# Optimization experiments

Hardware: AMD Instinct MI355X
Metric: run time of the kernel (lower is better)

## Reference

```python
import jax, jax.numpy as jnp
import numpy as np

B, F, E = 4096, 39, 16
FIELD_DIMS = [1000] * F
OFFSETS = jnp.asarray(np.concatenate([[0], np.cumsum(FIELD_DIMS)[:-1]]).astype(np.int64))
I_IDX, J_IDX = np.triu_indices(F, 1)  # 741 pairs (i<j)
I_IDX = jnp.asarray(I_IDX); J_IDX = jnp.asarray(J_IDX)
MLP_DIMS = [2 * 741 * E, 400, 400, 400]
EPS = 1e-5


def setup_inputs() -> dict:
    key = jax.random.key(0)
    ks = jax.random.split(key, 20)
    s = 0.02
    inp = {
        'x': jax.random.randint(ks[0], (B, F), 0, 1000, dtype=jnp.int64),
        'emb': jax.random.normal(ks[1], (sum(FIELD_DIMS), E), jnp.float32) * s,
        'sen_w1': jax.random.normal(ks[2], (F, F), jnp.float32) * s,
        'sen_b1': jnp.zeros((F,), jnp.float32),
        'sen_w2': jax.random.normal(ks[3], (F, F), jnp.float32) * s,
        'sen_b2': jnp.zeros((F,), jnp.float32),
        'Wb1': jax.random.normal(ks[4], (E, E), jnp.float32) * s,
        'Wb2': jax.random.normal(ks[5], (E, E), jnp.float32) * s,
    }
    for li in range(3):
        din, dout = MLP_DIMS[li], MLP_DIMS[li + 1]
        inp[f'mw{li}'] = jax.random.normal(ks[6 + li], (dout, din), jnp.float32) * s
        inp[f'mb{li}'] = jnp.zeros((dout,), jnp.float32)
        inp[f'g{li}'] = jnp.ones((dout,), jnp.float32)
        inp[f'be{li}'] = jnp.zeros((dout,), jnp.float32)
    inp['mw3'] = jax.random.normal(ks[9], (1, MLP_DIMS[-1]), jnp.float32) * s
    inp['mb3'] = jnp.zeros((1,), jnp.float32)
    return inp


def _bilinear_all(v, W):
    # v: [B,F,E]; p_ij = (v_i W^T) * v_j for all i<j -> [B, P*E]
    proj = jnp.einsum('bfe,de->bfd', v, W)
    p = proj[:, I_IDX] * v[:, J_IDX]  # [B, 741, E]
    return p.reshape(v.shape[0], -1)


def _bn(h, g, be):
    mu = h.mean(axis=0)
    var = h.var(axis=0)
    return g * (h - mu) * jax.lax.rsqrt(var + EPS) + be


def _forward(x, emb, sen_w1, sen_b1, sen_w2, sen_b2, Wb1, Wb2,
             mw0, mb0, g0, be0, mw1, mb1, g1, be1, mw2, mb2, g2, be2, mw3, mb3):
    xe = emb[x + OFFSETS[None, :]]  # [B,F,E]
    # SENet: max over embed dim, two-layer excitation with ReLU
    z = jnp.max(xe, axis=2)  # [B,F]
    a = jax.nn.relu(jax.nn.relu(z @ sen_w1.T + sen_b1) @ sen_w2.T + sen_b2)  # [B,F]
    x_sen = a[:, :, None] * xe
    x_con = jnp.concatenate([_bilinear_all(xe, Wb1), _bilinear_all(x_sen, Wb2)], axis=1)
    h = x_con
    for w, b, g, be in ((mw0, mb0, g0, be0), (mw1, mb1, g1, be1), (mw2, mb2, g2, be2)):
        h = jax.nn.relu(_bn(h @ w.T + b, g, be))  # dropout = identity (eval)
    return h @ mw3.T + mb3  # [B,1]


def reference(x, emb, sen_w1, sen_b1, sen_w2, sen_b2, Wb1, Wb2,
              mw0, mb0, g0, be0, mw1, mb1, g1, be1, mw2, mb2, g2, be2, mw3, mb3):
    return _forward(x, emb, sen_w1, sen_b1, sen_w2, sen_b2, Wb1, Wb2,
                    mw0, mb0, g0, be0, mw1, mb1, g1, be1, mw2, mb2, g2, be2, mw3, mb3)
```

## Files before the change

kernel.cpp:

```cpp
#include <hip/hip_runtime.h>
#include <stdint.h>

#define B_ROWS  4096
#define F_FIELDS 39
#define NPAIR   741
#define XCON_K  23712
#define KP      23744
#define NP      512
#define HID     400
#define SPLITK0 8
#define KITERS0 (KP/64)

#define OFF_XCON 0ull
#define SZ_XCON  ((size_t)B_ROWS * KP * 2)
#define OFF_W0B  (OFF_XCON + SZ_XCON)
#define SZ_W0B   ((size_t)NP * KP * 2)
#define OFF_W1B  (OFF_W0B + SZ_W0B)
#define SZ_WSM   ((size_t)NP * NP * 2)
#define OFF_W2B  (OFF_W1B + SZ_WSM)
#define OFF_HPRE (OFF_W2B + SZ_WSM)
#define SZ_HPRE  ((size_t)B_ROWS * NP * 4)
#define OFF_HN   (OFF_HPRE + SZ_HPRE)
#define SZ_HN    ((size_t)B_ROWS * NP * 2)
#define OFF_STATS (OFF_HN + SZ_HN)
#define SZ_STATS  (6 * 512 * 4)
#define WS_NEEDED (OFF_STATS + SZ_STATS + 4096)

__device__ __forceinline__ unsigned short f2bf(float f) {
    union { float f; unsigned u; } v; v.f = f;
    unsigned r = (v.u + 0x7FFFu + ((v.u >> 16) & 1u)) >> 16;
    return (unsigned short)r;
}
__device__ __forceinline__ float bf2f(unsigned short h) {
    union { unsigned u; float f; } v; v.u = ((unsigned)h) << 16;
    return v.f;
}
__device__ __forceinline__ void gl_lds16(const void* g, void* l) {
    __builtin_amdgcn_global_load_lds(
        (const __attribute__((address_space(1))) void*)g,
        (__attribute__((address_space(3))) void*)l, 16, 0, 0);
}

typedef __bf16 bf16x8 __attribute__((ext_vector_type(8)));
typedef float  floatx4 __attribute__((ext_vector_type(4)));

__global__ __launch_bounds__(256) void build_all(
    const int* __restrict__ x, const float* __restrict__ emb,
    const float* __restrict__ w1, const float* __restrict__ b1,
    const float* __restrict__ w2, const float* __restrict__ b2,
    const float* __restrict__ Wb1, const float* __restrict__ Wb2,
    unsigned short* __restrict__ xcon,
    const float* __restrict__ mw0, unsigned short* __restrict__ w0b,
    const float* __restrict__ mw1, const float* __restrict__ mw2,
    unsigned short* __restrict__ w1b, unsigned short* __restrict__ w2b)
{
    __shared__ float xe[624], p0[624], sp[624], sx[624];
    __shared__ float zz[40], tt[40], aa[40];
    __shared__ short itab[NPAIR], jtab[NPAIR];
    const int bb = blockIdx.x, tid = threadIdx.x;

    if (bb >= B_ROWS) {
        if (bb < B_ROWS + NP) {
            const int o = bb - B_ROWS;
            for (int k4 = tid; k4 < KP / 4; k4 += 256) {
                const int k = k4 * 4;
                unsigned short u[4] = {0, 0, 0, 0};
                if (o < HID && k < XCON_K) {
                    float4 v = *(const float4*)&mw0[(size_t)o * XCON_K + k];
                    u[0] = f2bf(v.x); u[1] = f2bf(v.y); u[2] = f2bf(v.z); u[3] = f2bf(v.w);
                }
                uint2 pk; pk.x = u[0] | ((unsigned)u[1] << 16); pk.y = u[2] | ((unsigned)u[3] << 16);
                *(uint2*)&w0b[(size_t)o * KP + k] = pk;
            }
        } else {
            const int idx = bb - B_ROWS - NP;
            const int which = idx >> 9;
            const int o = idx & 511;
            const float* w = which ? mw2 : mw1;
            unsigned short* o_ = which ? w2b : w1b;
            for (int k = tid; k < NP; k += 256) {
                float v = (o < HID && k < HID) ? w[o * HID + k] : 0.f;
                o_[o * NP + k] = f2bf(v);
            }
        }
        return;
    }

    const int b = bb;
    for (int p = tid; p < NPAIR; p += 256) {
        float fp = (float)p;
        int i = (int)(38.5f - sqrtf(38.5f * 38.5f - 2.f * fp));
        while (i > 0 && p < (i * (77 - i)) / 2) --i;
        while (p >= ((i + 1) * (76 - i)) / 2) ++i;
        itab[p] = (short)i;
        jtab[p] = (short)(i + 1 + (p - (i * (77 - i)) / 2));
    }
    if (tid < 156) {
        int f = tid >> 2, e4 = (tid & 3) * 4;
        int row = x[b * F_FIELDS + f] + 1000 * f;
        *(float4*)&xe[f * 16 + e4] = *(const float4*)&emb[row * 16 + e4];
    }
    __syncthreads();
    if (tid < F_FIELDS) {
        float m = xe[tid * 16];
        for (int e = 1; e < 16; ++e) m = fmaxf(m, xe[tid * 16 + e]);
        zz[tid] = m;
    }
    __syncthreads();
    if (tid < F_FIELDS) {
        float s = b1[tid];
        for (int g = 0; g < F_FIELDS; ++g) s += zz[g] * w1[tid * F_FIELDS + g];
        tt[tid] = fmaxf(s, 0.f);
    }
    __syncthreads();
    if (tid < F_FIELDS) {
        float s = b2[tid];
        for (int g = 0; g < F_FIELDS; ++g) s += tt[g] * w2[tid * F_FIELDS + g];
        aa[tid] = fmaxf(s, 0.f);
    }
    __syncthreads();
    for (int idx = tid; idx < 624; idx += 256) {
        int f = idx >> 4, d = idx & 15;
        float s1 = 0.f, s2 = 0.f;
        for (int e = 0; e < 16; ++e) {
            float v = xe[f * 16 + e];
            s1 += v * Wb1[d * 16 + e];
            s2 += v * Wb2[d * 16 + e];
        }
        const float af = aa[f];
        p0[idx] = s1;
        sp[idx] = af * s2;
        sx[idx] = af * xe[idx];
    }
    __syncthreads();
    unsigned short* out = xcon + (size_t)b * KP;
    for (int c = tid; c < 1484; c += 256) {
        if (c < 2 * NPAIR) {
            const int half = (c >= NPAIR);
            const int p = c - NPAIR * half;
            const int i = itab[p], j = jtab[p];
            const float* pr = half ? &sp[i * 16] : &p0[i * 16];
            const float* xr = half ? &sx[j * 16] : &xe[j * 16];
            unsigned short u[16];
#pragma unroll
            for (int q = 0; q < 4; ++q) {
                float4 a = *(const float4*)(pr + q * 4);
                float4 bx = *(const float4*)(xr + q * 4);
                u[q * 4 + 0] = f2bf(a.x * bx.x);
                u[q * 4 + 1] = f2bf(a.y * bx.y);
                u[q * 4 + 2] = f2bf(a.z * bx.z);
                u[q * 4 + 3] = f2bf(a.w * bx.w);
            }
            uint4 v0, v1;
            v0.x = u[0] | ((unsigned)u[1] << 16);  v0.y = u[2] | ((unsigned)u[3] << 16);
            v0.z = u[4] | ((unsigned)u[5] << 16);  v0.w = u[6] | ((unsigned)u[7] << 16);
            v1.x = u[8] | ((unsigned)u[9] << 16);  v1.y = u[10] | ((unsigned)u[11] << 16);
            v1.z = u[12] | ((unsigned)u[13] << 16); v1.w = u[14] | ((unsigned)u[15] << 16);
            uint4* dst = (uint4*)(out + (half ? 11856 : 0) + p * 16);
            dst[0] = v0; dst[1] = v1;
        } else {
            uint4 z; z.x = z.y = z.z = z.w = 0u;
            ((uint4*)(out + XCON_K))[c - 2 * NPAIR] = z;
        }
    }
}

__global__ __launch_bounds__(256, 2) void gemm0(
    const unsigned short* __restrict__ A, const unsigned short* __restrict__ Bm,
    float* __restrict__ C, int kcnt)
{
    __shared__ __align__(16) unsigned short As[128 * 64];
    __shared__ __align__(16) unsigned short Bs[256 * 64];
    const int tid = threadIdx.x;
    const int m0 = blockIdx.y * 128, n0 = blockIdx.x * 256;
    int kb = blockIdx.z * kcnt;
    int ke = kb + kcnt; if (ke > KITERS0) ke = KITERS0;

    const int swz = (((tid & 7) ^ ((tid >> 3) & 7)) * 8);
    const unsigned short* Ag = A + (size_t)(m0 + (tid >> 3)) * KP + swz;
    const unsigned short* Bg = Bm + (size_t)(n0 + (tid >> 3)) * KP + swz;
    unsigned short* Asl = As + tid * 8;
    unsigned short* Bsl = Bs + tid * 8;

    const int wv = tid >> 6, ln = tid & 63;
    const int wm = (wv >> 1) * 64, wn = (wv & 1) * 128;
    const int l15 = ln & 15, lq = ln >> 4;
    const int xorm = l15 & 7;

    floatx4 acc[4][8];
#pragma unroll
    for (int mi = 0; mi < 4; ++mi)
#pragma unroll
        for (int ni = 0; ni < 8; ++ni)
            acc[mi][ni] = (floatx4){0.f, 0.f, 0.f, 0.f};

    for (int kt = kb; kt < ke; ++kt) {
        const size_t ko = (size_t)kt * 64;
#pragma unroll
        for (int i = 0; i < 4; ++i)
            gl_lds16(Ag + (size_t)(i * 32) * KP + ko, Asl + i * 2048);
#pragma unroll
        for (int i = 0; i < 8; ++i)
            gl_lds16(Bg + (size_t)(i * 32) * KP + ko, Bsl + i * 2048);
        __syncthreads();
#pragma unroll
        for (int kk = 0; kk < 64; kk += 32) {
            bf16x8 af[4], bfr[8];
#pragma unroll
            for (int t = 0; t < 4; ++t)
                af[t] = *(const bf16x8*)(As + (wm + t * 16 + l15) * 64
                                            + ((((kk >> 3) + lq) ^ xorm) * 8));
#pragma unroll
            for (int t = 0; t < 8; ++t)
                bfr[t] = *(const bf16x8*)(Bs + (wn + t * 16 + l15) * 64
                                             + ((((kk >> 3) + lq) ^ xorm) * 8));
#pragma unroll
            for (int mi = 0; mi < 4; ++mi)
#pragma unroll
                for (int ni = 0; ni < 8; ++ni)
                    acc[mi][ni] = __builtin_amdgcn_mfma_f32_16x16x32_bf16(
                        af[mi], bfr[ni], acc[mi][ni], 0, 0, 0);
        }
        __syncthreads();
    }
#pragma unroll
    for (int mi = 0; mi < 4; ++mi)
#pragma unroll
        for (int ni = 0; ni < 8; ++ni) {
            const int col = n0 + wn + ni * 16 + l15;
            const int row0 = m0 + wm + mi * 16 + lq * 4;
#pragma unroll
            for (int r = 0; r < 4; ++r)
                atomicAdd(&C[(size_t)(row0 + r) * NP + col], acc[mi][ni][r]);
        }
}

template<int MODE>
__global__ __launch_bounds__(256) void gemm_bn(
    const void* __restrict__ Ain, const unsigned short* __restrict__ Bm,
    const float* __restrict__ cs, const float* __restrict__ csq,
    const float* __restrict__ g, const float* __restrict__ be,
    void* __restrict__ Cout, float* __restrict__ csO, float* __restrict__ csqO)
{
    __shared__ __align__(16) unsigned short As[64 * 64];
    __shared__ __align__(16) unsigned short Bs[64 * 64];
    __shared__ float sc[NP], sh[NP];
    const int tid = threadIdx.x;
    const int m0 = blockIdx.y * 64, n0 = blockIdx.x * 64;

    for (int c = tid; c < NP; c += 256) {
        float mean = cs[c] * (1.f / 4096.f);
        float var  = csq[c] * (1.f / 4096.f) - mean * mean;
        float s = (c < HID ? g[c] : 0.f) * rsqrtf(var + 1e-5f);
        sc[c] = s;
        sh[c] = (c < HID ? be[c] : 0.f) - mean * s;
    }

    const int r = tid >> 3, c8 = tid & 7;
    const int gsw = c8 ^ (r & 7);
    const unsigned short* Bg = Bm + (size_t)(n0 + r) * NP + gsw * 8;
    unsigned short* Bsl = Bs + tid * 8;

    const int wv = tid >> 6, ln = tid & 63;
    const int wm = (wv >> 1) * 32, wn = (wv & 1) * 32;
    const int l15 = ln & 15, lq = ln >> 4;
    const int xorm = l15 & 7;

    floatx4 acc[2][2];
#pragma unroll
    for (int mi = 0; mi < 2; ++mi)
#pragma unroll
        for (int ni = 0; ni < 2; ++ni)
            acc[mi][ni] = (floatx4){0.f, 0.f, 0.f, 0.f};

    __syncthreads();

    for (int kt = 0; kt < NP / 64; ++kt) {
        const int ko = kt * 64;
        const int kc = ko + gsw * 8;
#pragma unroll
        for (int i = 0; i < 2; ++i) {
            const int row = m0 + r + i * 32;
            unsigned short u[8];
            if (MODE == 0) {
                const float* ap = (const float*)Ain + (size_t)row * NP + kc;
                float4 v0 = *(const float4*)ap;
                float4 v1 = *(const float4*)(ap + 4);
                u[0] = f2bf(fmaxf(v0.x * sc[kc]     + sh[kc],     0.f));
                u[1] = f2bf(fmaxf(v0.y * sc[kc + 1] + sh[kc + 1], 0.f));
                u[2] = f2bf(fmaxf(v0.z * sc[kc + 2] + sh[kc + 2], 0.f));
                u[3] = f2bf(fmaxf(v0.w * sc[kc + 3] + sh[kc + 3], 0.f));
                u[4] = f2bf(fmaxf(v1.x * sc[kc + 4] + sh[kc + 4], 0.f));
                u[5] = f2bf(fmaxf(v1.y * sc[kc + 5] + sh[kc + 5], 0.f));
                u[6] = f2bf(fmaxf(v1.z * sc[kc + 6] + sh[kc + 6], 0.f));
                u[7] = f2bf(fmaxf(v1.w * sc[kc + 7] + sh[kc + 7], 0.f));
            } else {
                const unsigned short* ap = (const unsigned short*)Ain + (size_t)row * NP + kc;
                uint4 pk = *(const uint4*)ap;
                unsigned short raw[8] = {
                    (unsigned short)(pk.x & 0xFFFF), (unsigned short)(pk.x >> 16),
                    (unsigned short)(pk.y & 0xFFFF), (unsigned short)(pk.y >> 16),
                    (unsigned short)(pk.z & 0xFFFF), (unsigned short)(pk.z >> 16),
                    (unsigned short)(pk.w & 0xFFFF), (unsigned short)(pk.w >> 16)};
#pragma unroll
                for (int e = 0; e < 8; ++e)
                    u[e] = f2bf(fmaxf(bf2f(raw[e]) * sc[kc + e] + sh[kc + e], 0.f));
            }
            uint4 w;
            w.x = u[0] | ((unsigned)u[1] << 16);
            w.y = u[2] | ((unsigned)u[3] << 16);
            w.z = u[4] | ((unsigned)u[5] << 16);
            w.w = u[6] | ((unsigned)u[7] << 16);
            *(uint4*)(As + (r + i * 32) * 64 + c8 * 8) = w;
        }
#pragma unroll
        for (int i = 0; i < 2; ++i)
            gl_lds16(Bg + (size_t)(i * 32) * NP + ko, Bsl + i * 2048);
        __syncthreads();
#pragma unroll
        for (int kk = 0; kk < 64; kk += 32) {
            bf16x8 af[2], bfr[2];
#pragma unroll
            for (int t = 0; t < 2; ++t) {
                af[t]  = *(const bf16x8*)(As + (wm + t * 16 + l15) * 64
                                             + ((((kk >> 3) + lq) ^ xorm) * 8));
                bfr[t] = *(const bf16x8*)(Bs + (wn + t * 16 + l15) * 64
                                             + ((((kk >> 3) + lq) ^ xorm) * 8));
            }
#pragma unroll
            for (int mi = 0; mi < 2; ++mi)
#pragma unroll
                for (int ni = 0; ni < 2; ++ni)
                    acc[mi][ni] = __builtin_amdgcn_mfma_f32_16x16x32_bf16(
                        af[mi], bfr[ni], acc[mi][ni], 0, 0, 0);
        }
        __syncthreads();
    }
#pragma unroll
    for (int mi = 0; mi < 2; ++mi)
#pragma unroll
        for (int ni = 0; ni < 2; ++ni) {
            const int col = n0 + wn + ni * 16 + l15;
            const int row0 = m0 + wm + mi * 16 + lq * 4;
#pragma unroll
            for (int rr = 0; rr < 4; ++rr) {
                if (MODE == 0)
                    ((unsigned short*)Cout)[(size_t)(row0 + rr) * NP + col] = f2bf(acc[mi][ni][rr]);
                else
                    ((float*)Cout)[(size_t)(row0 + rr) * NP + col] = acc[mi][ni][rr];
            }
        }
#pragma unroll
    for (int ni = 0; ni < 2; ++ni) {
        float s = 0.f, q = 0.f;
#pragma unroll
        for (int mi = 0; mi < 2; ++mi)
#pragma unroll
            for (int rr = 0; rr < 4; ++rr) { float v = acc[mi][ni][rr]; s += v; q += v * v; }
        s += __shfl_down(s, 32); q += __shfl_down(q, 32);
        s += __shfl_down(s, 16); q += __shfl_down(q, 16);
        if (lq == 0) {
            const int col = n0 + wn + ni * 16 + l15;
            atomicAdd(&csO[col], s);
            atomicAdd(&csqO[col], q);
        }
    }
}

__global__ __launch_bounds__(256) void colstats(const float* __restrict__ H,
                                                float* __restrict__ cs, float* __restrict__ csq) {
    const int tid = threadIdx.x;
    const int c4 = (tid & 127) * 4;
    const int ro = tid >> 7;
    const int r0 = blockIdx.x * 32;
    float s0 = 0, s1 = 0, s2 = 0, s3 = 0, q0 = 0, q1 = 0, q2 = 0, q3 = 0;
#pragma unroll
    for (int i = 0; i < 16; ++i) {
        float4 v = *(const float4*)&H[(size_t)(r0 + ro + 2 * i) * NP + c4];
        s0 += v.x; q0 += v.x * v.x;  s1 += v.y; q1 += v.y * v.y;
        s2 += v.z; q2 += v.z * v.z;  s3 += v.w; q3 += v.w * v.w;
    }
    atomicAdd(&cs[c4], s0); atomicAdd(&cs[c4 + 1], s1);
    atomicAdd(&cs[c4 + 2], s2); atomicAdd(&cs[c4 + 3], s3);
    atomicAdd(&csq[c4], q0); atomicAdd(&csq[c4 + 1], q1);
    atomicAdd(&csq[c4 + 2], q2); atomicAdd(&csq[c4 + 3], q3);
}

__global__ __launch_bounds__(256) void bnrelu_dot(const float* __restrict__ H,
                       const float* __restrict__ cs, const float* __restrict__ csq,
                       const float* __restrict__ g, const float* __restrict__ be,
                       const float* __restrict__ w3, const float* __restrict__ b3,
                       float* __restrict__ out) {
    __shared__ float sc[NP], sh[NP], ww[NP];
    for (int c = threadIdx.x; c < NP; c += 256) {
        float mean = cs[c] * (1.f / 4096.f);
        float var  = csq[c] * (1.f / 4096.f) - mean * mean;
        float s = (c < HID ? g[c] : 0.f) * rsqrtf(var + 1e-5f);
        sc[c] = s;
        sh[c] = (c < HID ? be[c] : 0.f) - mean * s;
        ww[c] = (c < HID ? w3[c] : 0.f);
    }
    __syncthreads();
    const int wv = threadIdx.x >> 6, ln = threadIdx.x & 63;
    const int row = blockIdx.x * 4 + wv;
    const float4* hp = (const float4*)(H + (size_t)row * NP);
    float s = 0.f;
#pragma unroll
    for (int it = 0; it < 2; ++it) {
        const int c4 = it * 64 + ln;
        const int c = c4 * 4;
        float4 v = hp[c4];
        s += fmaxf(v.x * sc[c]     + sh[c],     0.f) * ww[c]
           + fmaxf(v.y * sc[c + 1] + sh[c + 1], 0.f) * ww[c + 1]
           + fmaxf(v.z * sc[c + 2] + sh[c + 2], 0.f) * ww[c + 2]
           + fmaxf(v.w * sc[c + 3] + sh[c + 3], 0.f) * ww[c + 3];
    }
#pragma unroll
    for (int o = 32; o; o >>= 1) s += __shfl_down(s, o);
    if (ln == 0) out[row] = s + b3[0];
}

extern "C" void kernel_launch(void* const* d_in, const int* in_sizes, int n_in,
                              void* d_out, int out_size, void* d_ws, size_t ws_size,
                              hipStream_t stream)
{
    const int*   x    = (const int*)d_in[0];
    const float* emb  = (const float*)d_in[1];
    const float* sw1  = (const float*)d_in[2];
    const float* sb1  = (const float*)d_in[3];
    const float* sw2  = (const float*)d_in[4];
    const float* sb2  = (const float*)d_in[5];
    const float* Wb1  = (const float*)d_in[6];
    const float* Wb2  = (const float*)d_in[7];
    const float* mw0  = (const float*)d_in[8];
    const float* g0   = (const float*)d_in[10];
    const float* be0  = (const float*)d_in[11];
    const float* mw1  = (const float*)d_in[12];
    const float* g1   = (const float*)d_in[14];
    const float* be1  = (const float*)d_in[15];
    const float* mw2  = (const float*)d_in[16];
    const float* g2   = (const float*)d_in[18];
    const float* be2  = (const float*)d_in[19];
    const float* mw3  = (const float*)d_in[20];
    const float* mb3  = (const float*)d_in[21];
    (void)in_sizes; (void)n_in; (void)out_size;
    if (ws_size < WS_NEEDED) return;

    char* ws = (char*)d_ws;
    unsigned short* xcon = (unsigned short*)(ws + OFF_XCON);
    unsigned short* w0b  = (unsigned short*)(ws + OFF_W0B);
    unsigned short* w1b  = (unsigned short*)(ws + OFF_W1B);
    unsigned short* w2b  = (unsigned short*)(ws + OFF_W2B);
    float* hpre = (float*)(ws + OFF_HPRE);
    unsigned short* hn = (unsigned short*)(ws + OFF_HN);
    float* stats = (float*)(ws + OFF_STATS);
    float* cs0 = stats,        *csq0 = stats + 512;
    float* cs1 = stats + 1024, *csq1 = stats + 1536;
    float* cs2 = stats + 2048, *csq2 = stats + 2560;

    build_all<<<B_ROWS + NP + 2 * NP, 256, 0, stream>>>(
        x, emb, sw1, sb1, sw2, sb2, Wb1, Wb2, xcon, mw0, w0b, mw1, mw2, w1b, w2b);

    hipMemsetAsync(hpre, 0, SZ_HPRE, stream);
    hipMemsetAsync(stats, 0, SZ_STATS, stream);

    gemm0<<<dim3(NP / 256, B_ROWS / 128, SPLITK0), 256, 0, stream>>>(
        xcon, w0b, hpre, (KITERS0 + SPLITK0 - 1) / SPLITK0);
    colstats<<<128, 256, 0, stream>>>(hpre, cs0, csq0);

    gemm_bn<0><<<dim3(NP / 64, B_ROWS / 64), 256, 0, stream>>>(
        hpre, w1b, cs0, csq0, g0, be0, hn, cs1, csq1);

    gemm_bn<1><<<dim3(NP / 64, B_ROWS / 64), 256, 0, stream>>>(
        hn, w2b, cs1, csq1, g1, be1, hpre, cs2, csq2);

    bnrelu_dot<<<B_ROWS / 4, 256, 0, stream>>>(hpre, cs2, csq2, g2, be2, mw3, mb3, (float*)d_out);
}
```

Before: 378.9 us.

## Write split-K partials to slabs and fuse reduction with column stats; pack rows per block

Split-K partial results of the first GEMM go to per-split slabs with plain stores, replacing the float atomics into a zeroed buffer. A new reduce_stats kernel sums the slabs, writes the result and accumulates the BN column statistics, so the hpre memset and separate colstats pass are dropped. The slab path only runs if the workspace is large enough and otherwise falls back to the old atomic path. Separately, build_all now handles four batch rows per block, one per wavefront, to cut block count and share the pair-index tables. The slabs add roughly 64MB of extra write and read traffic.

Result: slower. 403.4 us (+6.5%).

```diff
diff --git a/kernel.cpp b/kernel.cpp
--- a/kernel.cpp
+++ b/kernel.cpp
@@ -10,6 +10,7 @@
 #define HID     400
 #define SPLITK0 8
 #define KITERS0 (KP/64)
+#define NROWBLK (B_ROWS/4)
 
 #define OFF_XCON 0ull
 #define SZ_XCON  ((size_t)B_ROWS * KP * 2)
@@ -25,6 +26,10 @@
 #define OFF_STATS (OFF_HN + SZ_HN)
 #define SZ_STATS  (6 * 512 * 4)
 #define WS_NEEDED (OFF_STATS + SZ_STATS + 4096)
+#define OFF_PART  (OFF_STATS + SZ_STATS)
+#define SLAB_ELEMS ((size_t)B_ROWS * NP)
+#define SZ_PART   ((size_t)SPLITK0 * SLAB_ELEMS * 4)
+#define WS_BIG    (OFF_PART + SZ_PART + 4096)
 
 __device__ __forceinline__ unsigned short f2bf(float f) {
     union { float f; unsigned u; } v; v.f = f;
@@ -54,14 +59,11 @@
     const float* __restrict__ mw1, const float* __restrict__ mw2,
     unsigned short* __restrict__ w1b, unsigned short* __restrict__ w2b)
 {
-    __shared__ float xe[624], p0[624], sp[624], sx[624];
-    __shared__ float zz[40], tt[40], aa[40];
-    __shared__ short itab[NPAIR], jtab[NPAIR];
     const int bb = blockIdx.x, tid = threadIdx.x;
 
-    if (bb >= B_ROWS) {
-        if (bb < B_ROWS + NP) {
-            const int o = bb - B_ROWS;
+    if (bb >= NROWBLK) {
+        if (bb < NROWBLK + NP) {
+            const int o = bb - NROWBLK;
             for (int k4 = tid; k4 < KP / 4; k4 += 256) {
                 const int k = k4 * 4;
                 unsigned short u[4] = {0, 0, 0, 0};
@@ -73,7 +75,7 @@
                 *(uint2*)&w0b[(size_t)o * KP + k] = pk;
             }
         } else {
-            const int idx = bb - B_ROWS - NP;
+            const int idx = bb - NROWBLK - NP;
             const int which = idx >> 9;
             const int o = idx & 511;
             const float* w = which ? mw2 : mw1;
@@ -86,7 +88,12 @@
         return;
     }
 
-    const int b = bb;
+    __shared__ float xe[4][624], p0[4][624], sp[4][624], sx[4][624];
+    __shared__ float zz[4][40], tt[4][40], aa[4][40];
+    __shared__ short itab[NPAIR], jtab[NPAIR];
+    const int wv = tid >> 6, ln = tid & 63;
+    const int b = bb * 4 + wv;
+
     for (int p = tid; p < NPAIR; p += 256) {
         float fp = (float)p;
         int i = (int)(38.5f - sqrtf(38.5f * 38.5f - 2.f * fp));
@@ -95,52 +102,52 @@
         itab[p] = (short)i;
         jtab[p] = (short)(i + 1 + (p - (i * (77 - i)) / 2));
     }
-    if (tid < 156) {
-        int f = tid >> 2, e4 = (tid & 3) * 4;
+    for (int k = ln; k < 156; k += 64) {
+        int f = k >> 2, e4 = (k & 3) * 4;
         int row = x[b * F_FIELDS + f] + 1000 * f;
-        *(float4*)&xe[f * 16 + e4] = *(const float4*)&emb[row * 16 + e4];
-    }
-    __syncthreads();
-    if (tid < F_FIELDS) {
-        float m = xe[tid * 16];
-        for (int e = 1; e < 16; ++e) m = fmaxf(m, xe[tid * 16 + e]);
-        zz[tid] = m;
-    }
-    __syncthreads();
-    if (tid < F_FIELDS) {
-        float s = b1[tid];
-        for (int g = 0; g < F_FIELDS; ++g) s += zz[g] * w1[tid * F_FIELDS + g];
-        tt[tid] = fmaxf(s, 0.f);
-    }
-    __syncthreads();
-    if (tid < F_FIELDS) {
-        float s = b2[tid];
-        for (int g = 0; g < F_FIELDS; ++g) s += tt[g] * w2[tid * F_FIELDS + g];
-        aa[tid] = fmaxf(s, 0.f);
-    }
-    __syncthreads();
-    for (int idx = tid; idx < 624; idx += 256) {
+        *(float4*)&xe[wv][f * 16 + e4] = *(const float4*)&emb[row * 16 + e4];
+    }
+    __syncthreads();
+    if (ln < F_FIELDS) {
+        float m = xe[wv][ln * 16];
+        for (int e = 1; e < 16; ++e) m = fmaxf(m, xe[wv][ln * 16 + e]);
+        zz[wv][ln] = m;
+    }
+    __syncthreads();
+    if (ln < F_FIELDS) {
+        float s = b1[ln];
+        for (int g = 0; g < F_FIELDS; ++g) s += zz[wv][g] * w1[ln * F_FIELDS + g];
+        tt[wv][ln] = fmaxf(s, 0.f);
+    }
+    __syncthreads();
+    if (ln < F_FIELDS) {
+        float s = b2[ln];
+        for (int g = 0; g < F_FIELDS; ++g) s += tt[wv][g] * w2[ln * F_FIELDS + g];
+        aa[wv][ln] = fmaxf(s, 0.f);
+    }
+    __syncthreads();
+    for (int idx = ln; idx < 624; idx += 64) {
         int f = idx >> 4, d = idx & 15;
         float s1 = 0.f, s2 = 0.f;
         for (int e = 0; e < 16; ++e) {
-            float v = xe[f * 16 + e];
+            float v = xe[wv][f * 16 + e];
             s1 += v * Wb1[d * 16 + e];
             s2 += v * Wb2[d * 16 + e];
         }
-        const float af = aa[f];
-        p0[idx] = s1;
-        sp[idx] = af * s2;
-        sx[idx] = af * xe[idx];
+        const float af = aa[wv][f];
+        p0[wv][idx] = s1;
+        sp[wv][idx] = af * s2;
+        sx[wv][idx] = af * xe[wv][idx];
     }
     __syncthreads();
     unsigned short* out = xcon + (size_t)b * KP;
-    for (int c = tid; c < 1484; c += 256) {
+    for (int c = ln; c < 1484; c += 64) {
         if (c < 2 * NPAIR) {
             const int half = (c >= NPAIR);
             const int p = c - NPAIR * half;
             const int i = itab[p], j = jtab[p];
-            const float* pr = half ? &sp[i * 16] : &p0[i * 16];
-            const float* xr = half ? &sx[j * 16] : &xe[j * 16];
+            const float* pr = half ? &sp[wv][i * 16] : &p0[wv][i * 16];
+            const float* xr = half ? &sx[wv][j * 16] : &xe[wv][j * 16];
             unsigned short u[16];
 #pragma unroll
             for (int q = 0; q < 4; ++q) {
@@ -159,15 +166,15 @@
             uint4* dst = (uint4*)(out + (half ? 11856 : 0) + p * 16);
             dst[0] = v0; dst[1] = v1;
         } else {
-            uint4 z; z.x = z.y = z.z = z.w = 0u;
-            ((uint4*)(out + XCON_K))[c - 2 * NPAIR] = z;
+            uint4 z4; z4.x = z4.y = z4.z = z4.w = 0u;
+            ((uint4*)(out + XCON_K))[c - 2 * NPAIR] = z4;
         }
     }
 }
 
 __global__ __launch_bounds__(256, 2) void gemm0(
     const unsigned short* __restrict__ A, const unsigned short* __restrict__ Bm,
-    float* __restrict__ C, int kcnt)
+    float* __restrict__ C, float* __restrict__ Cslab, int kcnt, int use_slab)
 {
     __shared__ __align__(16) unsigned short As[128 * 64];
     __shared__ __align__(16) unsigned short Bs[256 * 64];
@@ -223,16 +230,75 @@
         }
         __syncthreads();
     }
-#pragma unroll
-    for (int mi = 0; mi < 4; ++mi)
-#pragma unroll
-        for (int ni = 0; ni < 8; ++ni) {
-            const int col = n0 + wn + ni * 16 + l15;
-            const int row0 = m0 + wm + mi * 16 + lq * 4;
-#pragma unroll
-            for (int r = 0; r < 4; ++r)
-                atomicAdd(&C[(size_t)(row0 + r) * NP + col], acc[mi][ni][r]);
-        }
+    if (use_slab) {
+        float* slab = Cslab + (size_t)blockIdx.z * SLAB_ELEMS;
+#pragma unroll
+        for (int mi = 0; mi < 4; ++mi)
+#pragma unroll
+            for (int ni = 0; ni < 8; ++ni) {
+                const int col = n0 + wn + ni * 16 + l15;
+                const int row0 = m0 + wm + mi * 16 + lq * 4;
+#pragma unroll
+                for (int r = 0; r < 4; ++r)
+                    slab[(size_t)(row0 + r) * NP + col] = acc[mi][ni][r];
+            }
+    } else {
+#pragma unroll
+        for (int mi = 0; mi < 4; ++mi)
+#pragma unroll
+            for (int ni = 0; ni < 8; ++ni) {
+                const int col = n0 + wn + ni * 16 + l15;
+                const int row0 = m0 + wm + mi * 16 + lq * 4;
+#pragma unroll
+                for (int r = 0; r < 4; ++r)
+                    atomicAdd(&C[(size_t)(row0 + r) * NP + col], acc[mi][ni][r]);
+            }
+    }
+}
+
+__global__ __launch_bounds__(256) void reduce_stats(const float* __restrict__ P,
+                        float* __restrict__ H, float* __restrict__ cs, float* __restrict__ csq) {
+    const int tid = threadIdx.x;
+    const int c4 = (tid & 127) * 4;
+    const int ro = tid >> 7;
+    const int r0 = blockIdx.x * 16;
+    float s0 = 0, s1 = 0, s2 = 0, s3 = 0, q0 = 0, q1 = 0, q2 = 0, q3 = 0;
+#pragma unroll
+    for (int i = 0; i < 8; ++i) {
+        const size_t off = (size_t)(r0 + ro + 2 * i) * NP + c4;
+        float4 a = *(const float4*)&P[off];
+#pragma unroll
+        for (int z = 1; z < SPLITK0; ++z) {
+            float4 b = *(const float4*)&P[(size_t)z * SLAB_ELEMS + off];
+            a.x += b.x; a.y += b.y; a.z += b.z; a.w += b.w;
+        }
+        *(float4*)&H[off] = a;
+        s0 += a.x; q0 += a.x * a.x;  s1 += a.y; q1 += a.y * a.y;
+        s2 += a.z; q2 += a.z * a.z;  s3 += a.w; q3 += a.w * a.w;
+    }
+    atomicAdd(&cs[c4], s0); atomicAdd(&cs[c4 + 1], s1);
+    atomicAdd(&cs[c4 + 2], s2); atomicAdd(&cs[c4 + 3], s3);
+    atomicAdd(&csq[c4], q0); atomicAdd(&csq[c4 + 1], q1);
+    atomicAdd(&csq[c4 + 2], q2); atomicAdd(&csq[c4 + 3], q3);
+}
+
+__global__ __launch_bounds__(256) void colstats(const float* __restrict__ H,
+                                                float* __restrict__ cs, float* __restrict__ csq) {
+    const int tid = threadIdx.x;
+    const int c4 = (tid & 127) * 4;
+    const int ro = tid >> 7;
+    const int r0 = blockIdx.x * 16;
+    float s0 = 0, s1 = 0, s2 = 0, s3 = 0, q0 = 0, q1 = 0, q2 = 0, q3 = 0;
+#pragma unroll
+    for (int i = 0; i < 8; ++i) {
+        float4 v = *(const float4*)&H[(size_t)(r0 + ro + 2 * i) * NP + c4];
+        s0 += v.x; q0 += v.x * v.x;  s1 += v.y; q1 += v.y * v.y;
+        s2 += v.z; q2 += v.z * v.z;  s3 += v.w; q3 += v.w * v.w;
+    }
+    atomicAdd(&cs[c4], s0); atomicAdd(&cs[c4 + 1], s1);
+    atomicAdd(&cs[c4 + 2], s2); atomicAdd(&cs[c4 + 3], s3);
+    atomicAdd(&csq[c4], q0); atomicAdd(&csq[c4 + 1], q1);
+    atomicAdd(&csq[c4 + 2], q2); atomicAdd(&csq[c4 + 3], q3);
 }
 
 template<int MODE>
@@ -365,25 +431,6 @@
             atomicAdd(&csqO[col], q);
         }
     }
-}
-
-__global__ __launch_bounds__(256) void colstats(const float* __restrict__ H,
-                                                float* __restrict__ cs, float* __restrict__ csq) {
-    const int tid = threadIdx.x;
-    const int c4 = (tid & 127) * 4;
-    const int ro = tid >> 7;
-    const int r0 = blockIdx.x * 32;
-    float s0 = 0, s1 = 0, s2 = 0, s3 = 0, q0 = 0, q1 = 0, q2 = 0, q3 = 0;
-#pragma unroll
-    for (int i = 0; i < 16; ++i) {
-        float4 v = *(const float4*)&H[(size_t)(r0 + ro + 2 * i) * NP + c4];
-        s0 += v.x; q0 += v.x * v.x;  s1 += v.y; q1 += v.y * v.y;
-        s2 += v.z; q2 += v.z * v.z;  s3 += v.w; q3 += v.w * v.w;
-    }
-    atomicAdd(&cs[c4], s0); atomicAdd(&cs[c4 + 1], s1);
-    atomicAdd(&cs[c4 + 2], s2); atomicAdd(&cs[c4 + 3], s3);
-    atomicAdd(&csq[c4], q0); atomicAdd(&csq[c4 + 1], q1);
-    atomicAdd(&csq[c4 + 2], q2); atomicAdd(&csq[c4 + 3], q3);
 }
 
 __global__ __launch_bounds__(256) void bnrelu_dot(const float* __restrict__ H,
@@ -445,6 +492,7 @@
     const float* mb3  = (const float*)d_in[21];
     (void)in_sizes; (void)n_in; (void)out_size;
     if (ws_size < WS_NEEDED) return;
+    const int use_slab = (ws_size >= WS_BIG) ? 1 : 0;
 
     char* ws = (char*)d_ws;
     unsigned short* xcon = (unsigned short*)(ws + OFF_XCON);
@@ -454,19 +502,26 @@
     float* hpre = (float*)(ws + OFF_HPRE);
     unsigned short* hn = (unsigned short*)(ws + OFF_HN);
     float* stats = (float*)(ws + OFF_STATS);
+    float* slab  = (float*)(ws + OFF_PART);
     float* cs0 = stats,        *csq0 = stats + 512;
     float* cs1 = stats + 1024, *csq1 = stats + 1536;
     float* cs2 = stats + 2048, *csq2 = stats + 2560;
 
-    build_all<<<B_ROWS + NP + 2 * NP, 256, 0, stream>>>(
+    build_all<<<NROWBLK + NP + 2 * NP, 256, 0, stream>>>(
         x, emb, sw1, sb1, sw2, sb2, Wb1, Wb2, xcon, mw0, w0b, mw1, mw2, w1b, w2b);
 
-    hipMemsetAsync(hpre, 0, SZ_HPRE, stream);
     hipMemsetAsync(stats, 0, SZ_STATS, stream);
 
-    gemm0<<<dim3(NP / 256, B_ROWS / 128, SPLITK0), 256, 0, stream>>>(
-        xcon, w0b, hpre, (KITERS0 + SPLITK0 - 1) / SPLITK0);
-    colstats<<<128, 256, 0, stream>>>(hpre, cs0, csq0);
+    if (use_slab) {
+        gemm0<<<dim3(NP / 256, B_ROWS / 128, SPLITK0), 256, 0, stream>>>(
+            xcon, w0b, hpre, slab, (KITERS0 + SPLITK0 - 1) / SPLITK0, 1);
+        reduce_stats<<<256, 256, 0, stream>>>(slab, hpre, cs0, csq0);
+    } else {
+        hipMemsetAsync(hpre, 0, SZ_HPRE, stream);
+        gemm0<<<dim3(NP / 256, B_ROWS / 128, SPLITK0), 256, 0, stream>>>(
+            xcon, w0b, hpre, slab, (KITERS0 + SPLITK0 - 1) / SPLITK0, 0);
+        colstats<<<256, 256, 0, stream>>>(hpre, cs0, csq0);
+    }
 
     gemm_bn<0><<<dim3(NP / 64, B_ROWS / 64), 256, 0, stream>>>(
         hpre, w1b, cs0, csq0, g0, be0, hn, cs1, csq1);
```

## Shrink gemm0 tile to 128x128, raise occupancy, split xcon stores per thread

Applied to the files above, without the earlier changes.

The main split-K GEMM tile shrinks from 128x256 to 128x128, with fewer accumulators per wave and launch bounds raised to 4 blocks per CU. The grid doubles in the N dimension, which should improve occupancy and load balance. In exchange each A tile is reloaded twice as often. The xcon build loop now has each thread write one 16-byte chunk, so stores are contiguous and the padding branch is folded in. colstats uses twice as many blocks, each covering half the rows.

New measurement: 424.1 us. 11.9% more time.

```diff
diff --git a/kernel.cpp b/kernel.cpp
--- a/kernel.cpp
+++ b/kernel.cpp
@@ -133,17 +133,20 @@
         sx[idx] = af * xe[idx];
     }
     __syncthreads();
-    unsigned short* out = xcon + (size_t)b * KP;
-    for (int c = tid; c < 1484; c += 256) {
-        if (c < 2 * NPAIR) {
-            const int half = (c >= NPAIR);
-            const int p = c - NPAIR * half;
+    uint4* out4 = (uint4*)(xcon + (size_t)b * KP);
+    for (int s = tid; s < 2968; s += 256) {
+        uint4 w;
+        if (s < 2964) {
+            const int p2 = s >> 1;
+            const int hi = s & 1;
+            const int half = (p2 >= NPAIR);
+            const int p = p2 - NPAIR * half;
             const int i = itab[p], j = jtab[p];
-            const float* pr = half ? &sp[i * 16] : &p0[i * 16];
-            const float* xr = half ? &sx[j * 16] : &xe[j * 16];
-            unsigned short u[16];
-#pragma unroll
-            for (int q = 0; q < 4; ++q) {
+            const float* pr = (half ? &sp[i * 16] : &p0[i * 16]) + hi * 8;
+            const float* xr = (half ? &sx[j * 16] : &xe[j * 16]) + hi * 8;
+            unsigned short u[8];
+#pragma unroll
+            for (int q = 0; q < 2; ++q) {
                 float4 a = *(const float4*)(pr + q * 4);
                 float4 bx = *(const float4*)(xr + q * 4);
                 u[q * 4 + 0] = f2bf(a.x * bx.x);
@@ -151,28 +154,25 @@
                 u[q * 4 + 2] = f2bf(a.z * bx.z);
                 u[q * 4 + 3] = f2bf(a.w * bx.w);
             }
-            uint4 v0, v1;
-            v0.x = u[0] | ((unsigned)u[1] << 16);  v0.y = u[2] | ((unsigned)u[3] << 16);
-            v0.z = u[4] | ((unsigned)u[5] << 16);  v0.w = u[6] | ((unsigned)u[7] << 16);
-            v1.x = u[8] | ((unsigned)u[9] << 16);  v1.y = u[10] | ((unsigned)u[11] << 16);
-            v1.z = u[12] | ((unsigned)u[13] << 16); v1.w = u[14] | ((unsigned)u[15] << 16);
-            uint4* dst = (uint4*)(out + (half ? 11856 : 0) + p * 16);
-            dst[0] = v0; dst[1] = v1;
+            w.x = u[0] | ((unsigned)u[1] << 16);
+            w.y = u[2] | ((unsigned)u[3] << 16);
+            w.z = u[4] | ((unsigned)u[5] << 16);
+            w.w = u[6] | ((unsigned)u[7] << 16);
         } else {
-            uint4 z; z.x = z.y = z.z = z.w = 0u;
-            ((uint4*)(out + XCON_K))[c - 2 * NPAIR] = z;
-        }
-    }
-}
-
-__global__ __launch_bounds__(256, 2) void gemm0(
+            w.x = w.y = w.z = w.w = 0u;
+        }
+        out4[s] = w;
+    }
+}
+
+__global__ __launch_bounds__(256, 4) void gemm0(
     const unsigned short* __restrict__ A, const unsigned short* __restrict__ Bm,
     float* __restrict__ C, int kcnt)
 {
     __shared__ __align__(16) unsigned short As[128 * 64];
-    __shared__ __align__(16) unsigned short Bs[256 * 64];
+    __shared__ __align__(16) unsigned short Bs[128 * 64];
     const int tid = threadIdx.x;
-    const int m0 = blockIdx.y * 128, n0 = blockIdx.x * 256;
+    const int m0 = blockIdx.y * 128, n0 = blockIdx.x * 128;
     int kb = blockIdx.z * kcnt;
     int ke = kb + kcnt; if (ke > KITERS0) ke = KITERS0;
 
@@ -183,15 +183,15 @@
     unsigned short* Bsl = Bs + tid * 8;
 
     const int wv = tid >> 6, ln = tid & 63;
-    const int wm = (wv >> 1) * 64, wn = (wv & 1) * 128;
+    const int wm = (wv >> 1) * 64, wn = (wv & 1) * 64;
     const int l15 = ln & 15, lq = ln >> 4;
     const int xorm = l15 & 7;
 
-    floatx4 acc[4][8];
+    floatx4 acc[4][4];
 #pragma unroll
     for (int mi = 0; mi < 4; ++mi)
 #pragma unroll
-        for (int ni = 0; ni < 8; ++ni)
+        for (int ni = 0; ni < 4; ++ni)
             acc[mi][ni] = (floatx4){0.f, 0.f, 0.f, 0.f};
 
     for (int kt = kb; kt < ke; ++kt) {
@@ -200,24 +200,23 @@
         for (int i = 0; i < 4; ++i)
             gl_lds16(Ag + (size_t)(i * 32) * KP + ko, Asl + i * 2048);
 #pragma unroll
-        for (int i = 0; i < 8; ++i)
+        for (int i = 0; i < 4; ++i)
             gl_lds16(Bg + (size_t)(i * 32) * KP + ko, Bsl + i * 2048);
         __syncthreads();
 #pragma unroll
         for (int kk = 0; kk < 64; kk += 32) {
-            bf16x8 af[4], bfr[8];
-#pragma unroll
-            for (int t = 0; t < 4; ++t)
-                af[t] = *(const bf16x8*)(As + (wm + t * 16 + l15) * 64
-                                            + ((((kk >> 3) + lq) ^ xorm) * 8));
-#pragma unroll
-            for (int t = 0; t < 8; ++t)
+            bf16x8 af[4], bfr[4];
+#pragma unroll
+            for (int t = 0; t < 4; ++t) {
+                af[t]  = *(const bf16x8*)(As + (wm + t * 16 + l15) * 64
+                                             + ((((kk >> 3) + lq) ^ xorm) * 8));
                 bfr[t] = *(const bf16x8*)(Bs + (wn + t * 16 + l15) * 64
                                              + ((((kk >> 3) + lq) ^ xorm) * 8));
+            }
 #pragma unroll
             for (int mi = 0; mi < 4; ++mi)
 #pragma unroll
-                for (int ni = 0; ni < 8; ++ni)
+                for (int ni = 0; ni < 4; ++ni)
                     acc[mi][ni] = __builtin_amdgcn_mfma_f32_16x16x32_bf16(
                         af[mi], bfr[ni], acc[mi][ni], 0, 0, 0);
         }
@@ -226,13 +225,32 @@
 #pragma unroll
     for (int mi = 0; mi < 4; ++mi)
 #pragma unroll
-        for (int ni = 0; ni < 8; ++ni) {
+        for (int ni = 0; ni < 4; ++ni) {
             const int col = n0 + wn + ni * 16 + l15;
             const int row0 = m0 + wm + mi * 16 + lq * 4;
 #pragma unroll
             for (int r = 0; r < 4; ++r)
                 atomicAdd(&C[(size_t)(row0 + r) * NP + col], acc[mi][ni][r]);
         }
+}
+
+__global__ __launch_bounds__(256) void colstats(const float* __restrict__ H,
+                                                float* __restrict__ cs, float* __restrict__ csq) {
+    const int tid = threadIdx.x;
+    const int c4 = (tid & 127) * 4;
+    const int ro = tid >> 7;
+    const int r0 = blockIdx.x * 16;
+    float s0 = 0, s1 = 0, s2 = 0, s3 = 0, q0 = 0, q1 = 0, q2 = 0, q3 = 0;
+#pragma unroll
+    for (int i = 0; i < 8; ++i) {
+        float4 v = *(const float4*)&H[(size_t)(r0 + ro + 2 * i) * NP + c4];
+        s0 += v.x; q0 += v.x * v.x;  s1 += v.y; q1 += v.y * v.y;
+        s2 += v.z; q2 += v.z * v.z;  s3 += v.w; q3 += v.w * v.w;
+    }
+    atomicAdd(&cs[c4], s0); atomicAdd(&cs[c4 + 1], s1);
+    atomicAdd(&cs[c4 + 2], s2); atomicAdd(&cs[c4 + 3], s3);
+    atomicAdd(&csq[c4], q0); atomicAdd(&csq[c4 + 1], q1);
+    atomicAdd(&csq[c4 + 2], q2); atomicAdd(&csq[c4 + 3], q3);
 }
 
 template<int MODE>
@@ -365,25 +383,6 @@
             atomicAdd(&csqO[col], q);
         }
     }
-}
-
-__global__ __launch_bounds__(256) void colstats(const float* __restrict__ H,
-                                                float* __restrict__ cs, float* __restrict__ csq) {
-    const int tid = threadIdx.x;
-    const int c4 = (tid & 127) * 4;
-    const int ro = tid >> 7;
-    const int r0 = blockIdx.x * 32;
-    float s0 = 0, s1 = 0, s2 = 0, s3 = 0, q0 = 0, q1 = 0, q2 = 0, q3 = 0;
-#pragma unroll
-    for (int i = 0; i < 16; ++i) {
-        float4 v = *(const float4*)&H[(size_t)(r0 + ro + 2 * i) * NP + c4];
-        s0 += v.x; q0 += v.x * v.x;  s1 += v.y; q1 += v.y * v.y;
-        s2 += v.z; q2 += v.z * v.z;  s3 += v.w; q3 += v.w * v.w;
-    }
-    atomicAdd(&cs[c4], s0); atomicAdd(&cs[c4 + 1], s1);
-    atomicAdd(&cs[c4 + 2], s2); atomicAdd(&cs[c4 + 3], s3);
-    atomicAdd(&csq[c4], q0); atomicAdd(&csq[c4 + 1], q1);
-    atomicAdd(&csq[c4 + 2], q2); atomicAdd(&csq[c4 + 3], q3);
 }
 
 __global__ __launch_bounds__(256) void bnrelu_dot(const float* __restrict__ H,
@@ -464,9 +463,9 @@
     hipMemsetAsync(hpre, 0, SZ_HPRE, stream);
     hipMemsetAsync(stats, 0, SZ_STATS, stream);
 
-    gemm0<<<dim3(NP / 256, B_ROWS / 128, SPLITK0), 256, 0, stream>>>(
+    gemm0<<<dim3(NP / 128, B_ROWS / 128, SPLITK0), 256, 0, stream>>>(
         xcon, w0b, hpre, (KITERS0 + SPLITK0 - 1) / SPLITK0);
-    colstats<<<128, 256, 0, stream>>>(hpre, cs0, csq0);
+    colstats<<<256, 256, 0, stream>>>(hpre, cs0, csq0);
 
     gemm_bn<0><<<dim3(NP / 64, B_ROWS / 64), 256, 0, stream>>>(
         hpre, w1b, cs0, csq0, g0, be0, hn, cs1, csq1);
```
